# Kernel tuning notes

Hardware: AMD Instinct MI355X
Metric: run time of the kernel (lower is better)

The kernel has to match this reference:

```python
import jax, jax.numpy as jnp
import numpy as np

E = 1024   # embed_dim
H = 16     # num_heads
D = E // H # head_dim = 64
B = 2
S = 2048

def setup_inputs() -> dict:
    key = jax.random.key(0)
    ks = jax.random.split(key, 11)
    std = 0.02
    return {
        "query": jax.random.normal(ks[0], (B, S, E), jnp.float32),
        "key":   jax.random.normal(ks[1], (B, S, E), jnp.float32),
        "value": jax.random.normal(ks[2], (B, S, E), jnp.float32),
        "Wq": std * jax.random.normal(ks[3], (E, E), jnp.float32),
        "bq": jnp.zeros((E,), jnp.float32),
        "Wk": std * jax.random.normal(ks[4], (D, E), jnp.float32),
        "bk": jnp.zeros((D,), jnp.float32),
        "Wv": std * jax.random.normal(ks[5], (D, E), jnp.float32),
        "bv": jnp.zeros((D,), jnp.float32),
        "Wo": std * jax.random.normal(ks[6], (E, E), jnp.float32),
        "bo": jnp.zeros((E,), jnp.float32),
    }

def reference(query, key, value, Wq, bq, Wk, bk, Wv, bv, Wo, bo):
    b, t, _ = query.shape
    scaling = D ** -0.5
    q = query @ Wq.T + bq                      # [B, T, E]
    k = key @ Wk.T + bk                        # [B, S, D] (single shared KV head)
    v = value @ Wv.T + bv                      # [B, S, D]
    q = q.reshape(b, t, H, D).transpose(0, 2, 1, 3) * scaling  # [B, H, T, D]
    # MQA: broadcast shared k/v across heads inside einsum (no materialized expand)
    attn_weights = jnp.einsum("bhtd,bsd->bhts", q, k)          # [B, H, T, S]
    attn_probs = jax.nn.softmax(attn_weights, axis=-1)
    attn_output = jnp.einsum("bhts,bsd->bhtd", attn_probs, v)  # [B, H, T, D]
    attn_output = attn_output.transpose(0, 2, 1, 3).reshape(b, t, E)
    return attn_output @ Wo.T + bo
```

## Files before the change

kernel.cpp:

```cpp
#include <hip/hip_runtime.h>

#define E_DIM  1024
#define H_HEADS 16
#define D_HEAD  64
#define B_BATCH 2
#define S_SEQ  2048
#define M_ROWS (B_BATCH * S_SEQ)

typedef unsigned short u16;
typedef unsigned int   u32;
typedef __attribute__((ext_vector_type(8))) short bf16x8;
typedef __attribute__((ext_vector_type(4))) short bf16x4;
typedef __attribute__((ext_vector_type(4))) float f32x4;

#define MFMA32(a, b, c) __builtin_amdgcn_mfma_f32_16x16x32_bf16(a, b, c, 0, 0, 0)

#if __has_builtin(__builtin_amdgcn_mfma_f32_16x16x16bf16_1k)
#define HAVE_MFMA16 1
#define MFMA16(a, b, c) __builtin_amdgcn_mfma_f32_16x16x16bf16_1k(a, b, c, 0, 0, 0)
#else
#define HAVE_MFMA16 0
#endif

__device__ __forceinline__ u16 f2bf(float f) {
    union { float f; u32 i; } x; x.f = f;
    u32 r = x.i + 0x7fffu + ((x.i >> 16) & 1u);
    return (u16)(r >> 16);
}

#if __has_builtin(__builtin_amdgcn_cvt_pk_bf16_f32)
typedef __attribute__((ext_vector_type(2))) __bf16 bfp2;
__device__ __forceinline__ u32 pk2(float a, float b) {
    bfp2 t = __builtin_amdgcn_cvt_pk_bf16_f32(a, b);
    union { bfp2 v; u32 u; } c; c.v = t; return c.u;
}
#else
__device__ __forceinline__ u32 pk2(float a, float b) {
    return (u32)f2bf(a) | ((u32)f2bf(b) << 16);
}
#endif

__device__ __forceinline__ bf16x8 cvt8(const float4& a, const float4& b) {
    union { u32 u[4]; bf16x8 v; } t;
    t.u[0] = pk2(a.x, a.y); t.u[1] = pk2(a.z, a.w);
    t.u[2] = pk2(b.x, b.y); t.u[3] = pk2(b.z, b.w);
    return t.v;
}
__device__ __forceinline__ bf16x4 pack4(const f32x4& v) {
    union { u32 u[2]; bf16x4 w; } t;
    t.u[0] = pk2(v[0], v[1]); t.u[1] = pk2(v[2], v[3]);
    return t.w;
}

__device__ __forceinline__ void gl_lds16(const u16* g, u16* l) {
    __builtin_amdgcn_global_load_lds(
        (const __attribute__((address_space(1))) u32*)g,
        (__attribute__((address_space(3))) u32*)l, 16, 0, 0);
}

__global__ __launch_bounds__(256) void prep_kernel(
    const float* __restrict__ query, const float* __restrict__ Wq,
    const float* __restrict__ Wo,
    u16* __restrict__ qc, u16* __restrict__ wq_bf, u16* __restrict__ wo_bf,
    const float* __restrict__ key, const float* __restrict__ value,
    const float* __restrict__ Wk, const float* __restrict__ Wv,
    const float* __restrict__ bk, const float* __restrict__ bv,
    u16* __restrict__ Kout, u16* __restrict__ VTout, int M, int K)
{
    __shared__ u16 Asm[2][64 * 32];
    __shared__ u16 Bsm[2][64 * 32];

    const int bid = blockIdx.x;
    const int tid = threadIdx.x;

    if (bid >= 128) {
        const int cbid = bid - 128;
        const float* src; u16* dst; size_t base;
        if (cbid < 2048)      { src = query; dst = qc;    base = (size_t)cbid * 2048; }
        else if (cbid < 2560) { src = Wq;    dst = wq_bf; base = (size_t)(cbid - 2048) * 2048; }
        else                  { src = Wo;    dst = wo_bf; base = (size_t)(cbid - 2560) * 2048; }
        const size_t i = base + (size_t)tid * 8;
        float4 a = ((const float4*)(src + i))[0];
        float4 b = ((const float4*)(src + i))[1];
        *(bf16x8*)(dst + i) = cvt8(a, b);
        return;
    }

    const bool vproj = (bid >= 64);
    const float* A    = vproj ? value : key;
    const float* W    = vproj ? Wv : Wk;
    const float* bias = vproj ? bv : bk;

    const int w  = tid >> 6;
    const int ln = tid & 63;
    const int n  = ln & 15;
    const int qd = ln >> 4;
    const int wm = (w & 1) * 32;
    const int wn = (w >> 1) * 32;
    const int m0 = (bid & 63) * 64;

    const int srow = tid >> 2;
    const int scol = (tid & 3) * 8;

    f32x4 acc[2][2];
#pragma unroll
    for (int mt = 0; mt < 2; mt++)
#pragma unroll
        for (int nt = 0; nt < 2; nt++) acc[mt][nt] = (f32x4){0.f, 0.f, 0.f, 0.f};

    float4 a0, a1, w0, w1;
    auto loadT = [&](int k0) {
        const float* pa = A + (size_t)(m0 + srow) * K + k0 + scol;
        const float* pw = W + (size_t)srow * K + k0 + scol;
        a0 = ((const float4*)pa)[0]; a1 = ((const float4*)pa)[1];
        w0 = ((const float4*)pw)[0]; w1 = ((const float4*)pw)[1];
    };

    const int nk = K / 32;
    loadT(0);
    *(bf16x8*)&Asm[0][srow * 32 + scol] = cvt8(a0, a1);
    *(bf16x8*)&Bsm[0][srow * 32 + scol] = cvt8(w0, w1);

    for (int t = 0; t < nk; ++t) {
        if (t + 1 < nk) loadT((t + 1) * 32);
        __syncthreads();

        bf16x8 af[2], bfr[2];
#pragma unroll
        for (int t2 = 0; t2 < 2; t2++) {
            af[t2]  = *(const bf16x8*)&Asm[t & 1][(wm + t2 * 16 + n) * 32 + qd * 8];
            bfr[t2] = *(const bf16x8*)&Bsm[t & 1][(wn + t2 * 16 + n) * 32 + qd * 8];
        }
#pragma unroll
        for (int mt = 0; mt < 2; mt++)
#pragma unroll
            for (int nt = 0; nt < 2; nt++)
                acc[mt][nt] = MFMA32(af[mt], bfr[nt], acc[mt][nt]);

        if (t + 1 < nk) {
            *(bf16x8*)&Asm[(t + 1) & 1][srow * 32 + scol] = cvt8(a0, a1);
            *(bf16x8*)&Bsm[(t + 1) & 1][srow * 32 + scol] = cvt8(w0, w1);
        }
    }

    if (!vproj) {
#pragma unroll
        for (int mt = 0; mt < 2; mt++)
#pragma unroll
            for (int r = 0; r < 4; r++) {
                const int row = m0 + wm + mt * 16 + qd * 4 + r;
#pragma unroll
                for (int nt = 0; nt < 2; nt++) {
                    const int col = wn + nt * 16 + n;
                    Kout[(size_t)row * 64 + col] = f2bf(acc[mt][nt][r] + bias[col]);
                }
            }
    } else {
#pragma unroll
        for (int mt = 0; mt < 2; mt++)
#pragma unroll
            for (int nt = 0; nt < 2; nt++) {
                const int col = wn + nt * 16 + n;
                const int row0 = m0 + wm + mt * 16 + qd * 4;
                float b4 = bias[col];
                ushort4 pk;
                pk.x = f2bf(acc[mt][nt][0] + b4);
                pk.y = f2bf(acc[mt][nt][1] + b4);
                pk.z = f2bf(acc[mt][nt][2] + b4);
                pk.w = f2bf(acc[mt][nt][3] + b4);
                *(ushort4*)&VTout[(size_t)col * M + row0] = pk;
            }
    }
}

template<bool OUT_BF16>
__global__ __launch_bounds__(256, 2) void gemm_bf16_kernel(
    const u16* __restrict__ A, const u16* __restrict__ W,
    const float* __restrict__ bias, void* __restrict__ Cv,
    int M, int N, int K, float scale)
{
    __shared__ u16 Asm[3][2][128 * 32];
    __shared__ u16 Bsm[3][2][64 * 32];

    const int tid = threadIdx.x;
    const int w  = tid >> 6;
    const int ln = tid & 63;
    const int n  = ln & 15;
    const int qd = ln >> 4;
    const int ns = (n & 3) ^ (n >> 2);
    const int wm = (w & 1) * 64;
    const int wn = (w >> 1) * 32;

    const int m0 = blockIdx.y * 128;
    const int n0 = blockIdx.x * 64;

    const int srow = tid >> 2;
    const int sblk = tid & 3;
    const int sc   = ((sblk ^ (srow & 3) ^ ((srow >> 2) & 3)) * 8);

    f32x4 acc[4][2];
#pragma unroll
    for (int mt = 0; mt < 4; mt++)
#pragma unroll
        for (int nt = 0; nt < 2; nt++) acc[mt][nt] = (f32x4){0.f, 0.f, 0.f, 0.f};

    auto stage = [&](int p, int k0) {
#pragma unroll
        for (int kb = 0; kb < 2; kb++)
#pragma unroll
            for (int g = 0; g < 2; g++) {
                const int row = g * 64 + srow;
                gl_lds16(A + (size_t)(m0 + row) * K + k0 + kb * 32 + sc,
                         &Asm[p][kb][row * 32 + sblk * 8]);
            }
#pragma unroll
        for (int kb = 0; kb < 2; kb++)
            gl_lds16(W + (size_t)(n0 + srow) * K + k0 + kb * 32 + sc,
                     &Bsm[p][kb][srow * 32 + sblk * 8]);
    };
    auto compute = [&](int p) {
        bf16x8 af[4][2], bfr[2][2];
#pragma unroll
        for (int kb = 0; kb < 2; kb++) {
#pragma unroll
            for (int mt = 0; mt < 4; mt++) {
                const int r = wm + mt * 16 + n;
                af[mt][kb] = *(const bf16x8*)&Asm[p][kb][r * 32 + ((qd ^ ns) * 8)];
            }
#pragma unroll
            for (int nt = 0; nt < 2; nt++) {
                const int r = wn + nt * 16 + n;
                bfr[nt][kb] = *(const bf16x8*)&Bsm[p][kb][r * 32 + ((qd ^ ns) * 8)];
            }
        }
#pragma unroll
        for (int kb = 0; kb < 2; kb++)
#pragma unroll
            for (int mt = 0; mt < 4; mt++)
#pragma unroll
                for (int nt = 0; nt < 2; nt++)
                    acc[mt][nt] = MFMA32(af[mt][kb], bfr[nt][kb], acc[mt][nt]);
    };

    const int nt_tiles = K / 64;
    stage(0, 0);
    stage(1, 64);

    int pc = 0, ps = 2;
    for (int t = 0; t + 2 < nt_tiles; ++t) {
        asm volatile("s_waitcnt vmcnt(6)" ::: "memory");
        __builtin_amdgcn_s_barrier();
        __builtin_amdgcn_sched_barrier(0);
        stage(ps, (t + 2) * 64);
        compute(pc);
        pc = (pc == 2) ? 0 : pc + 1;
        ps = (ps == 2) ? 0 : ps + 1;
    }
    asm volatile("s_waitcnt vmcnt(6)" ::: "memory");
    __builtin_amdgcn_s_barrier();
    __builtin_amdgcn_sched_barrier(0);
    compute(pc);
    pc = (pc == 2) ? 0 : pc + 1;
    asm volatile("s_waitcnt vmcnt(0)" ::: "memory");
    __builtin_amdgcn_s_barrier();
    __builtin_amdgcn_sched_barrier(0);
    compute(pc);

    float bb[2];
#pragma unroll
    for (int nt = 0; nt < 2; nt++) bb[nt] = bias[n0 + wn + nt * 16 + n] * scale;

#pragma unroll
    for (int mt = 0; mt < 4; mt++)
#pragma unroll
        for (int r = 0; r < 4; r++) {
            const int row = m0 + wm + mt * 16 + qd * 4 + r;
#pragma unroll
            for (int nt = 0; nt < 2; nt++) {
                const int col = n0 + wn + nt * 16 + n;
                float v = acc[mt][nt][r] * scale + bb[nt];
                if (OUT_BF16) ((u16*)Cv)[(size_t)row * N + col] = f2bf(v);
                else        ((float*)Cv)[(size_t)row * N + col] = v;
            }
        }
}

__global__ __launch_bounds__(256, 2) void mqa_attn_mfma_kernel(
    const u16* Q, const u16* __restrict__ K,
    const u16* __restrict__ VT, u16* O)
{
    __shared__ u16 ksm[2][2][128 * 32];
    __shared__ u16 vsm[2][4][64 * 32];
#if !HAVE_MFMA16
    __shared__ u16 psm[4][32 * 128];
#endif

    const int tid = threadIdx.x;
    const int w   = tid >> 6;
    const int ln  = tid & 63;
    const int n   = ln & 15;
    const int qd  = ln >> 4;
    const int lr  = ln >> 2;
    const int blk = ln & 3;
    const int ns  = (n & 3) ^ (n >> 2);
    const int rs  = (lr & 3) ^ (lr >> 2);

    const int bid = blockIdx.x;
    const int qb = bid & 15;
    const int h  = (bid >> 4) & (H_HEADS - 1);
    const int b  = bid >> 8;
    const int q0 = qb * 128;

    const u16* kg = K  + (size_t)b * S_SEQ * 64;
    const u16* vg = VT + (size_t)b * S_SEQ;

    auto stageKV = [&](int p, int s0) {
#pragma unroll
        for (int kb = 0; kb < 2; kb++)
#pragma unroll
            for (int j = 0; j < 2; j++) {
                int row = w * 32 + j * 16 + lr;
                gl_lds16(kg + (size_t)(s0 + row) * 64 + kb * 32 + ((blk ^ rs) * 8),
                         &ksm[p][kb][row * 32 + blk * 8]);
            }
#pragma unroll
        for (int j = 0; j < 4; j++) {
            int d = j * 16 + lr;
            gl_lds16(vg + (size_t)d * M_ROWS + s0 + w * 32 + ((blk ^ rs) * 8),
                     &vsm[p][w][d * 32 + blk * 8]);
        }
    };

    {
        const u16* qg = Q + (size_t)(b * S_SEQ + q0) * E_DIM + h * 64;
#pragma unroll
        for (int kb = 0; kb < 2; kb++)
#pragma unroll
            for (int j = 0; j < 2; j++) {
                int row = w * 32 + j * 16 + lr;
                gl_lds16(qg + (size_t)row * E_DIM + kb * 32 + ((blk ^ rs) * 8),
                         &ksm[1][kb][row * 32 + blk * 8]);
            }
    }
    __syncthreads();

    bf16x8 qa[2][2];
#pragma unroll
    for (int mt = 0; mt < 2; mt++)
#pragma unroll
        for (int kb = 0; kb < 2; kb++) {
            int row = w * 32 + mt * 16 + n;
            qa[mt][kb] = *(const bf16x8*)&ksm[1][kb][row * 32 + ((qd ^ ns) * 8)];
        }

    stageKV(0, 0);

    f32x4 acc_o[2][4];
    float lsum[2] = {0.f, 0.f};
#pragma unroll
    for (int mt = 0; mt < 2; mt++)
#pragma unroll
        for (int ntd = 0; ntd < 4; ntd++) acc_o[mt][ntd] = (f32x4){0.f, 0.f, 0.f, 0.f};

    int p = 0;
    for (int s0 = 0; s0 < S_SEQ; s0 += 128) {
        __syncthreads();
        if (s0 + 128 < S_SEQ) stageKV(p ^ 1, s0 + 128);

        f32x4 sacc[2][8];
#pragma unroll
        for (int mt = 0; mt < 2; mt++)
#pragma unroll
            for (int nt = 0; nt < 8; nt++) sacc[mt][nt] = (f32x4){0.f, 0.f, 0.f, 0.f};
#pragma unroll
        for (int nt = 0; nt < 8; nt++) {
            int rowk = nt * 16 + n;
#pragma unroll
            for (int kb = 0; kb < 2; kb++) {
                bf16x8 kf = *(const bf16x8*)&ksm[p][kb][rowk * 32 + ((qd ^ ns) * 8)];
                sacc[0][nt] = MFMA32(kf, qa[0][kb], sacc[0][nt]);
                sacc[1][nt] = MFMA32(kf, qa[1][kb], sacc[1][nt]);
            }
        }

        bf16x4 pa[2][8];
#pragma unroll
        for (int mt = 0; mt < 2; mt++) {
            float ls = 0.f;
#pragma unroll
            for (int nt = 0; nt < 8; nt++) {
#pragma unroll
                for (int r = 0; r < 4; r++) {
                    float pv = exp2f(sacc[mt][nt][r]);
                    sacc[mt][nt][r] = pv;
                    ls += pv;
                }
                pa[mt][nt] = pack4(sacc[mt][nt]);
            }
            lsum[mt] += ls;
        }

#if HAVE_MFMA16
#pragma unroll
        for (int kk = 0; kk < 8; kk++) {
            int c = kk >> 1;
            int lblk = (kk & 1) * 2 + (qd >> 1);
#pragma unroll
            for (int ntd = 0; ntd < 4; ntd++) {
                int d = ntd * 16 + n;
                bf16x4 bv = *(const bf16x4*)
                    &vsm[p][c][d * 32 + ((lblk ^ ns) * 8) + (qd & 1) * 4];
                acc_o[0][ntd] = MFMA16(pa[0][kk], bv, acc_o[0][ntd]);
                acc_o[1][ntd] = MFMA16(pa[1][kk], bv, acc_o[1][ntd]);
            }
        }
#else
#pragma unroll
        for (int mt = 0; mt < 2; mt++)
#pragma unroll
            for (int nt = 0; nt < 8; nt++) {
                int t = mt * 16 + n;
                int lb = nt * 2 + (qd >> 1);
                union { bf16x4 v; uint2 u; } pw; pw.v = pa[mt][nt];
                *(uint2*)&psm[w][t * 128 + ((lb ^ n) * 8) + (qd & 1) * 4] = pw.u;
            }
        __syncthreads();
#pragma unroll
        for (int kb = 0; kb < 4; kb++) {
            bf16x8 paf[2];
#pragma unroll
            for (int mt = 0; mt < 2; mt++) {
                int t = mt * 16 + n;
                paf[mt] = *(const bf16x8*)&psm[w][t * 128 + (((kb * 4 + qd) ^ n) * 8)];
            }
#pragma unroll
            for (int ntd = 0; ntd < 4; ntd++) {
                int d = ntd * 16 + n;
                bf16x8 bv = *(const bf16x8*)&vsm[p][kb][d * 32 + ((qd ^ ns) * 8)];
                acc_o[0][ntd] = MFMA32(paf[0], bv, acc_o[0][ntd]);
                acc_o[1][ntd] = MFMA32(paf[1], bv, acc_o[1][ntd]);
            }
        }
#endif
        p ^= 1;
    }

#pragma unroll
    for (int mt = 0; mt < 2; mt++) {
        lsum[mt] += __shfl_xor(lsum[mt], 16);
        lsum[mt] += __shfl_xor(lsum[mt], 32);
    }
#pragma unroll
    for (int mt = 0; mt < 2; mt++)
#pragma unroll
        for (int r = 0; r < 4; r++) {
            float inv = 1.f / __shfl(lsum[mt], qd * 4 + r);
            int grow = b * S_SEQ + q0 + w * 32 + mt * 16 + qd * 4 + r;
#pragma unroll
            for (int ntd = 0; ntd < 4; ntd++) {
                int gcol = h * D_HEAD + ntd * 16 + n;
                O[(size_t)grow * E_DIM + gcol] = f2bf(acc_o[mt][ntd][r] * inv);
            }
        }
}

extern "C" void kernel_launch(void* const* d_in, const int* in_sizes, int n_in,
                              void* d_out, int out_size, void* d_ws, size_t ws_size,
                              hipStream_t stream) {
    const float* query = (const float*)d_in[0];
    const float* key   = (const float*)d_in[1];
    const float* value = (const float*)d_in[2];
    const float* Wq    = (const float*)d_in[3];
    const float* bq    = (const float*)d_in[4];
    const float* Wk    = (const float*)d_in[5];
    const float* bk    = (const float*)d_in[6];
    const float* Wv    = (const float*)d_in[7];
    const float* bv    = (const float*)d_in[8];
    const float* Wo    = (const float*)d_in[9];
    const float* bo    = (const float*)d_in[10];
    float* out = (float*)d_out;

    const int M = M_ROWS;

    u16* q_bf  = (u16*)d_ws;
    u16* k_bf  = q_bf + (size_t)M * E_DIM;
    u16* vt_bf = k_bf + (size_t)M * D_HEAD;
    u16* wq_bf = vt_bf + (size_t)M * D_HEAD;
    u16* wo_bf = wq_bf + (size_t)E_DIM * E_DIM;

    u16* qc_bf = (u16*)d_out;

    dim3 blk(256);
    const float scaling = 0.125f * 1.44269504088896f;

    prep_kernel<<<dim3(3200), blk, 0, stream>>>(
        query, Wq, Wo, qc_bf, wq_bf, wo_bf,
        key, value, Wk, Wv, bk, bv, k_bf, vt_bf, M, E_DIM);

    gemm_bf16_kernel<true><<<dim3(E_DIM / 64, M / 128), blk, 0, stream>>>(
        qc_bf, wq_bf, bq, q_bf, M, E_DIM, E_DIM, scaling);

    mqa_attn_mfma_kernel<<<dim3(B_BATCH * H_HEADS * (S_SEQ / 128)), blk, 0, stream>>>(
        q_bf, k_bf, vt_bf, q_bf);

    gemm_bf16_kernel<false><<<dim3(E_DIM / 64, M / 128), blk, 0, stream>>>(
        q_bf, wo_bf, bo, out, M, E_DIM, E_DIM, 1.0f);
}
```

Baseline: 249.8 us.

## Fuse Q projection GEMM into MQA attention kernel

After: 235.5 us. -5.7%, faster.

```diff
diff --git a/kernel.cpp b/kernel.cpp
--- a/kernel.cpp
+++ b/kernel.cpp
@@ -285,12 +285,13 @@
         }
 }
 
-__global__ __launch_bounds__(256, 2) void mqa_attn_mfma_kernel(
-    const u16* Q, const u16* __restrict__ K,
-    const u16* __restrict__ VT, u16* O)
+__global__ __launch_bounds__(256, 2) void mqa_attn_fused_kernel(
+    const u16* __restrict__ QC, const u16* __restrict__ WQ,
+    const float* __restrict__ bq,
+    const u16* __restrict__ Kt, const u16* __restrict__ VT,
+    u16* __restrict__ O, float scaling)
 {
-    __shared__ u16 ksm[2][2][128 * 32];
-    __shared__ u16 vsm[2][4][64 * 32];
+    __shared__ u16 lds[32768];
 #if !HAVE_MFMA16
     __shared__ u16 psm[4][32 * 128];
 #endif
@@ -311,47 +312,119 @@
     const int b  = bid >> 8;
     const int q0 = qb * 128;
 
-    const u16* kg = K  + (size_t)b * S_SEQ * 64;
+    const u16* ag = QC + (size_t)(b * S_SEQ + q0) * E_DIM;
+    const u16* wg = WQ + (size_t)(h * 64) * E_DIM;
+
+    const int srow = tid >> 2;
+    const int sblk = tid & 3;
+    const int sc   = ((sblk ^ (srow & 3) ^ ((srow >> 2) & 3)) * 8);
+
+    auto stageP1 = [&](int buf, int k0) {
+        u16* pa = lds + buf * 12288;
+        u16* pb = pa + 8192;
+#pragma unroll
+        for (int kb = 0; kb < 2; kb++)
+#pragma unroll
+            for (int g = 0; g < 2; g++) {
+                const int row = g * 64 + srow;
+                gl_lds16(ag + (size_t)row * E_DIM + k0 + kb * 32 + sc,
+                         pa + kb * 4096 + row * 32 + sblk * 8);
+            }
+#pragma unroll
+        for (int kb = 0; kb < 2; kb++)
+            gl_lds16(wg + (size_t)srow * E_DIM + k0 + kb * 32 + sc,
+                     pb + kb * 2048 + srow * 32 + sblk * 8);
+    };
+
+    float bqv[4];
+#pragma unroll
+    for (int nt = 0; nt < 4; nt++) bqv[nt] = bq[h * 64 + nt * 16 + n] * scaling;
+
+    f32x4 qacc[2][4];
+#pragma unroll
+    for (int mt = 0; mt < 2; mt++)
+#pragma unroll
+        for (int nt = 0; nt < 4; nt++) qacc[mt][nt] = (f32x4){0.f, 0.f, 0.f, 0.f};
+
+    stageP1(0, 0);
+    for (int t = 0; t < 16; ++t) {
+        __syncthreads();
+        if (t + 1 < 16) stageP1((t + 1) & 1, (t + 1) * 64);
+        const u16* pa = lds + (t & 1) * 12288;
+        const u16* pb = pa + 8192;
+        bf16x8 af[2][2], bfr[4][2];
+#pragma unroll
+        for (int kb = 0; kb < 2; kb++) {
+#pragma unroll
+            for (int mt = 0; mt < 2; mt++) {
+                const int r = w * 32 + mt * 16 + n;
+                af[mt][kb] = *(const bf16x8*)&pa[kb * 4096 + r * 32 + ((qd ^ ns) * 8)];
+            }
+#pragma unroll
+            for (int nt = 0; nt < 4; nt++) {
+                const int r = nt * 16 + n;
+                bfr[nt][kb] = *(const bf16x8*)&pb[kb * 2048 + r * 32 + ((qd ^ ns) * 8)];
+            }
+        }
+#pragma unroll
+        for (int kb = 0; kb < 2; kb++)
+#pragma unroll
+            for (int mt = 0; mt < 2; mt++)
+#pragma unroll
+                for (int nt = 0; nt < 4; nt++)
+                    qacc[mt][nt] = MFMA32(af[mt][kb], bfr[nt][kb], qacc[mt][nt]);
+    }
+
+    {
+        u16* qsm = lds + 24576;
+#pragma unroll
+        for (int mt = 0; mt < 2; mt++)
+#pragma unroll
+            for (int r = 0; r < 4; r++) {
+                const int row = w * 32 + mt * 16 + qd * 4 + r;
+                const int rsw = (row & 3) ^ ((row >> 2) & 3);
+#pragma unroll
+                for (int nt = 0; nt < 4; nt++) {
+                    const int col = nt * 16 + n;
+                    float v = qacc[mt][nt][r] * scaling + bqv[nt];
+                    const int kb = col >> 5, c = col & 31;
+                    qsm[kb * 4096 + row * 32 + (((c >> 3) ^ rsw) * 8) + (c & 7)] = f2bf(v);
+                }
+            }
+    }
+    __syncthreads();
+
+    bf16x8 qa[2][2];
+#pragma unroll
+    for (int mt = 0; mt < 2; mt++)
+#pragma unroll
+        for (int kb = 0; kb < 2; kb++) {
+            const int row = w * 32 + mt * 16 + n;
+            qa[mt][kb] = *(const bf16x8*)&lds[24576 + kb * 4096 + row * 32 + ((qd ^ ns) * 8)];
+        }
+
+    const u16* kg = Kt + (size_t)b * S_SEQ * 64;
     const u16* vg = VT + (size_t)b * S_SEQ;
 
+    auto KSM = [&](int p, int kb) -> u16* { return lds + ((p * 2 + kb) * 4096); };
+    auto VSM = [&](int p, int c)  -> u16* { return lds + 16384 + ((p * 4 + c) * 2048); };
+
     auto stageKV = [&](int p, int s0) {
 #pragma unroll
         for (int kb = 0; kb < 2; kb++)
 #pragma unroll
             for (int j = 0; j < 2; j++) {
-                int row = w * 32 + j * 16 + lr;
+                const int row = w * 32 + j * 16 + lr;
                 gl_lds16(kg + (size_t)(s0 + row) * 64 + kb * 32 + ((blk ^ rs) * 8),
-                         &ksm[p][kb][row * 32 + blk * 8]);
+                         KSM(p, kb) + row * 32 + blk * 8);
             }
 #pragma unroll
         for (int j = 0; j < 4; j++) {
-            int d = j * 16 + lr;
+            const int d = j * 16 + lr;
             gl_lds16(vg + (size_t)d * M_ROWS + s0 + w * 32 + ((blk ^ rs) * 8),
-                     &vsm[p][w][d * 32 + blk * 8]);
+                     VSM(p, w) + d * 32 + blk * 8);
         }
     };
-
-    {
-        const u16* qg = Q + (size_t)(b * S_SEQ + q0) * E_DIM + h * 64;
-#pragma unroll
-        for (int kb = 0; kb < 2; kb++)
-#pragma unroll
-            for (int j = 0; j < 2; j++) {
-                int row = w * 32 + j * 16 + lr;
-                gl_lds16(qg + (size_t)row * E_DIM + kb * 32 + ((blk ^ rs) * 8),
-                         &ksm[1][kb][row * 32 + blk * 8]);
-            }
-    }
-    __syncthreads();
-
-    bf16x8 qa[2][2];
-#pragma unroll
-    for (int mt = 0; mt < 2; mt++)
-#pragma unroll
-        for (int kb = 0; kb < 2; kb++) {
-            int row = w * 32 + mt * 16 + n;
-            qa[mt][kb] = *(const bf16x8*)&ksm[1][kb][row * 32 + ((qd ^ ns) * 8)];
-        }
 
     stageKV(0, 0);
 
@@ -374,10 +447,10 @@
             for (int nt = 0; nt < 8; nt++) sacc[mt][nt] = (f32x4){0.f, 0.f, 0.f, 0.f};
 #pragma unroll
         for (int nt = 0; nt < 8; nt++) {
-            int rowk = nt * 16 + n;
+            const int rowk = nt * 16 + n;
 #pragma unroll
             for (int kb = 0; kb < 2; kb++) {
-                bf16x8 kf = *(const bf16x8*)&ksm[p][kb][rowk * 32 + ((qd ^ ns) * 8)];
+                bf16x8 kf = *(const bf16x8*)&KSM(p, kb)[rowk * 32 + ((qd ^ ns) * 8)];
                 sacc[0][nt] = MFMA32(kf, qa[0][kb], sacc[0][nt]);
                 sacc[1][nt] = MFMA32(kf, qa[1][kb], sacc[1][nt]);
             }
@@ -403,13 +476,13 @@
 #if HAVE_MFMA16
 #pragma unroll
         for (int kk = 0; kk < 8; kk++) {
-            int c = kk >> 1;
-            int lblk = (kk & 1) * 2 + (qd >> 1);
+            const int c = kk >> 1;
+            const int lblk = (kk & 1) * 2 + (qd >> 1);
 #pragma unroll
             for (int ntd = 0; ntd < 4; ntd++) {
-                int d = ntd * 16 + n;
+                const int d = ntd * 16 + n;
                 bf16x4 bv = *(const bf16x4*)
-                    &vsm[p][c][d * 32 + ((lblk ^ ns) * 8) + (qd & 1) * 4];
+                    &VSM(p, c)[d * 32 + ((lblk ^ ns) * 8) + (qd & 1) * 4];
                 acc_o[0][ntd] = MFMA16(pa[0][kk], bv, acc_o[0][ntd]);
                 acc_o[1][ntd] = MFMA16(pa[1][kk], bv, acc_o[1][ntd]);
             }
@@ -419,8 +492,8 @@
         for (int mt = 0; mt < 2; mt++)
 #pragma unroll
             for (int nt = 0; nt < 8; nt++) {
-                int t = mt * 16 + n;
-                int lb = nt * 2 + (qd >> 1);
+                const int t = mt * 16 + n;
+                const int lb = nt * 2 + (qd >> 1);
                 union { bf16x4 v; uint2 u; } pw; pw.v = pa[mt][nt];
                 *(uint2*)&psm[w][t * 128 + ((lb ^ n) * 8) + (qd & 1) * 4] = pw.u;
             }
@@ -430,13 +503,13 @@
             bf16x8 paf[2];
 #pragma unroll
             for (int mt = 0; mt < 2; mt++) {
-                int t = mt * 16 + n;
+                const int t = mt * 16 + n;
                 paf[mt] = *(const bf16x8*)&psm[w][t * 128 + (((kb * 4 + qd) ^ n) * 8)];
             }
 #pragma unroll
             for (int ntd = 0; ntd < 4; ntd++) {
-                int d = ntd * 16 + n;
-                bf16x8 bv = *(const bf16x8*)&vsm[p][kb][d * 32 + ((qd ^ ns) * 8)];
+                const int d = ntd * 16 + n;
+                bf16x8 bv = *(const bf16x8*)&VSM(p, kb)[d * 32 + ((qd ^ ns) * 8)];
                 acc_o[0][ntd] = MFMA32(paf[0], bv, acc_o[0][ntd]);
                 acc_o[1][ntd] = MFMA32(paf[1], bv, acc_o[1][ntd]);
             }
@@ -455,10 +528,10 @@
 #pragma unroll
         for (int r = 0; r < 4; r++) {
             float inv = 1.f / __shfl(lsum[mt], qd * 4 + r);
-            int grow = b * S_SEQ + q0 + w * 32 + mt * 16 + qd * 4 + r;
+            const int grow = b * S_SEQ + q0 + w * 32 + mt * 16 + qd * 4 + r;
 #pragma unroll
             for (int ntd = 0; ntd < 4; ntd++) {
-                int gcol = h * D_HEAD + ntd * 16 + n;
+                const int gcol = h * D_HEAD + ntd * 16 + n;
                 O[(size_t)grow * E_DIM + gcol] = f2bf(acc_o[mt][ntd][r] * inv);
             }
         }
@@ -497,11 +570,8 @@
         query, Wq, Wo, qc_bf, wq_bf, wo_bf,
         key, value, Wk, Wv, bk, bv, k_bf, vt_bf, M, E_DIM);
 
-    gemm_bf16_kernel<true><<<dim3(E_DIM / 64, M / 128), blk, 0, stream>>>(
-        qc_bf, wq_bf, bq, q_bf, M, E_DIM, E_DIM, scaling);
-
-    mqa_attn_mfma_kernel<<<dim3(B_BATCH * H_HEADS * (S_SEQ / 128)), blk, 0, stream>>>(
-        q_bf, k_bf, vt_bf, q_bf);
+    mqa_attn_fused_kernel<<<dim3(512), blk, 0, stream>>>(
+        qc_bf, wq_bf, bq, k_bf, vt_bf, q_bf, scaling);
 
     gemm_bf16_kernel<false><<<dim3(E_DIM / 64, M / 128), blk, 0, stream>>>(
         q_bf, wo_bf, bo, out, M, E_DIM, E_DIM, 1.0f);
```
